# Optimization experiments

Hardware: AMD Instinct MI355X
Metric: run time of the kernel (lower is better)

## Reference

```python
import jax, jax.numpy as jnp
import numpy as np


def _gcn_conv(x, W, b, src, dst, norm, n_nodes):
    # PyG GCNConv: h = x @ W, then symmetric-normalized aggregation, then + b
    h = x @ W                                   # [N, F_out]
    msg = h[src] * norm[:, None]                # gather + scale, [E', F_out]
    agg = jax.ops.segment_sum(msg, dst, num_segments=n_nodes)
    return agg + b


def _norm_and_loops(edge_index, n_nodes):
    # add self-loops, compute D^{-1/2} (A+I) D^{-1/2} edge weights
    loop = jnp.arange(n_nodes, dtype=edge_index.dtype)
    src = jnp.concatenate([edge_index[0], loop])
    dst = jnp.concatenate([edge_index[1], loop])
    deg = jax.ops.segment_sum(jnp.ones_like(dst, dtype=jnp.float32), dst,
                              num_segments=n_nodes)
    dinv = jnp.where(deg > 0, jax.lax.rsqrt(deg), 0.0)
    norm = dinv[src] * dinv[dst]
    return src, dst, norm


def setup_inputs() -> dict:
    key = jax.random.key(0)
    ks = jax.random.split(key, 4)
    N, E, n_latent, n_dim = 50000, 800000, 128, 128
    hidden = 2 * n_latent
    x = jax.random.normal(ks[0], (N, n_latent), dtype=jnp.float32)
    edge_index = jax.random.randint(ks[1], (2, E), 0, N, dtype=jnp.int64)
    W1 = jax.random.normal(ks[2], (n_latent, hidden), dtype=jnp.float32) / np.sqrt(n_latent)
    b1 = jnp.zeros((hidden,), dtype=jnp.float32)
    W2 = jax.random.normal(ks[3], (hidden, n_dim), dtype=jnp.float32) / np.sqrt(hidden)
    b2 = jnp.zeros((n_dim,), dtype=jnp.float32)
    return {"x": x, "edge_index": edge_index, "W1": W1, "b1": b1,
            "W2": W2, "b2": b2}


def reference(x, edge_index, W1, b1, W2, b2):
    n_nodes = x.shape[0]
    src, dst, norm = _norm_and_loops(edge_index, n_nodes)
    z1 = jax.nn.relu(_gcn_conv(x, W1, b1, src, dst, norm, n_nodes))
    z2 = _gcn_conv(z1, W2, b2, src, dst, norm, n_nodes)
    return z2
```

## Files before the change

### kernel.cpp

```cpp
#include <hip/hip_runtime.h>


constexpr int F = 128;
constexpr int HID = 256;
constexpr int ECHUNK = 8192;

typedef __attribute__((ext_vector_type(8))) short bf16x8;
typedef __attribute__((ext_vector_type(4))) float f32x4;

__device__ inline unsigned short f2bf(float f) {
  unsigned u = __float_as_uint(f);
  u += 0x7fffu + ((u >> 16) & 1u);
  return (unsigned short)(u >> 16);
}
__device__ inline float bf2f(unsigned short s) {
  return __uint_as_float(((unsigned)s) << 16);
}

__global__ __launch_bounds__(256) void k_bzero(unsigned* bcnt) {
  bcnt[threadIdx.x] = 0u;
}

__global__ __launch_bounds__(256) void k_binc(const int* __restrict__ dst,
                                              unsigned* __restrict__ bcnt, int E) {
  __shared__ unsigned hist[256];
  int tid = threadIdx.x;
  hist[tid] = 0u;
  __syncthreads();
  int i0 = blockIdx.x * ECHUNK;
  int i1 = min(i0 + ECHUNK, E);
  for (int i = i0 + tid; i < i1; i += 256)
    atomicAdd(&hist[((unsigned)dst[i]) >> 8], 1u);
  __syncthreads();
  unsigned c = hist[tid];
  if (c) atomicAdd(&bcnt[tid], c);
}

__global__ __launch_bounds__(256) void k_bscan(const unsigned* __restrict__ bcnt,
                                               unsigned* __restrict__ bbase,
                                               unsigned* __restrict__ bcur,
                                               int* __restrict__ rowptr,
                                               int P, int N, int E) {
  __shared__ unsigned wsum[4];
  int tid = threadIdx.x;
  unsigned v = (tid < P) ? bcnt[tid] : 0u;
  unsigned sv = v;
#pragma unroll
  for (int off = 1; off < 64; off <<= 1) {
    unsigned t = __shfl_up(sv, off);
    if ((tid & 63) >= off) sv += t;
  }
  int w = tid >> 6;
  if ((tid & 63) == 63) wsum[w] = sv;
  __syncthreads();
  unsigned wpre = 0;
  for (int k = 0; k < w; ++k) wpre += wsum[k];
  unsigned excl = wpre + sv - v;
  if (tid < P) {
    bbase[tid] = excl;
    bcur[tid] = excl;
  }
  if (tid == P - 1) bbase[P] = excl + v;
  if (tid == 0) rowptr[N] = E;
}

__global__ __launch_bounds__(256) void k_binscat(const int* __restrict__ src,
                                                 const int* __restrict__ dst,
                                                 unsigned* __restrict__ bcur,
                                                 unsigned* __restrict__ packed, int E) {
  __shared__ unsigned hist[256];
  __shared__ unsigned basel[256];
  int tid = threadIdx.x;
  hist[tid] = 0u;
  __syncthreads();
  int i0 = blockIdx.x * ECHUNK;
  int i1 = min(i0 + ECHUNK, E);
  for (int i = i0 + tid; i < i1; i += 256)
    atomicAdd(&hist[((unsigned)dst[i]) >> 8], 1u);
  __syncthreads();
  unsigned c = hist[tid];
  if (c) basel[tid] = atomicAdd(&bcur[tid], c);
  __syncthreads();
  hist[tid] = 0u;
  __syncthreads();
  for (int i = i0 + tid; i < i1; i += 256) {
    unsigned d = (unsigned)dst[i];
    unsigned b = d >> 8;
    unsigned pos = basel[b] + atomicAdd(&hist[b], 1u);
    packed[pos] = ((unsigned)src[i]) | ((d & 255u) << 16);
  }
}

__global__ __launch_bounds__(256) void k_bcsr(const unsigned* __restrict__ packed,
                                              const unsigned* __restrict__ bbase,
                                              unsigned* __restrict__ deg,
                                              int* __restrict__ rowptr,
                                              int* __restrict__ esrc, int N) {
  __shared__ unsigned hist[256];
  __shared__ unsigned rowloc[256];
  __shared__ unsigned cur[256];
  __shared__ unsigned wsum[4];
  int tid = threadIdx.x, b = blockIdx.x;
  int e0 = (int)bbase[b], e1 = (int)bbase[b + 1];
  hist[tid] = 0u;
  __syncthreads();
  for (int i = e0 + tid; i < e1; i += 256)
    atomicAdd(&hist[packed[i] >> 16], 1u);
  __syncthreads();
  unsigned v = hist[tid];
  unsigned sv = v;
#pragma unroll
  for (int off = 1; off < 64; off <<= 1) {
    unsigned t = __shfl_up(sv, off);
    if ((tid & 63) >= off) sv += t;
  }
  int w = tid >> 6;
  if ((tid & 63) == 63) wsum[w] = sv;
  __syncthreads();
  unsigned wpre = 0;
  for (int k = 0; k < w; ++k) wpre += wsum[k];
  unsigned excl = wpre + sv - v;
  int node = b * 256 + tid;
  if (node < N) {
    deg[node] = v;
    rowptr[node] = e0 + (int)excl;
  }
  rowloc[tid] = (unsigned)e0 + excl;
  cur[tid] = 0u;
  __syncthreads();
  for (int i = e0 + tid; i < e1; i += 256) {
    unsigned pk = packed[i];
    unsigned dl = pk >> 16;
    unsigned pos = rowloc[dl] + atomicAdd(&cur[dl], 1u);
    esrc[pos] = (int)(pk & 0xffffu);
  }
}

__global__ __launch_bounds__(256) void k_dinv(const unsigned* __restrict__ deg,
                                              float* dinv, int N) {
  int i = blockIdx.x * 256 + threadIdx.x;
  if (i < N) dinv[i] = rsqrtf((float)deg[i] + 1.0f);
}

__global__ __launch_bounds__(256) void k_tobf(const float* __restrict__ in,
                                              unsigned short* __restrict__ outp,
                                              int n4) {
  int i = blockIdx.x * 256 + threadIdx.x;
  if (i >= n4) return;
  float4 v = ((const float4*)in)[i];
  ushort4 o;
  o.x = f2bf(v.x); o.y = f2bf(v.y); o.z = f2bf(v.z); o.w = f2bf(v.w);
  ((ushort4*)outp)[i] = o;
}

__global__ __launch_bounds__(256) void k_wsplit(const float* __restrict__ W,
                                                unsigned short* __restrict__ hi,
                                                unsigned short* __restrict__ lo,
                                                int K, int Nn) {
  int idx = blockIdx.x * 256 + threadIdx.x;
  if (idx >= K * Nn) return;
  int k = idx / Nn, n = idx - k * Nn;
  float f = W[idx];
  unsigned short h = f2bf(f);
  unsigned short l = f2bf(f - bf2f(h));
  hi[n * K + k] = h;
  lo[n * K + k] = l;
}

__global__ __launch_bounds__(256) void k_agg_bf(const int* __restrict__ rowptr,
                                                const int* __restrict__ esrc,
                                                const float* __restrict__ dinv,
                                                const float* __restrict__ xf,
                                                const unsigned short* __restrict__ xb,
                                                unsigned short* __restrict__ outh,
                                                unsigned short* __restrict__ outl,
                                                int N) {
  int node = blockIdx.x * 4 + (threadIdx.x >> 6);
  int lane = threadIdx.x & 63;
  if (node >= N) return;
  float di = dinv[node];
  float w0 = di * di;
  float2 acc = ((const float2*)(xf + (size_t)node * F))[lane];
  acc.x *= w0; acc.y *= w0;
  int beg = rowptr[node], end = rowptr[node + 1];
  for (int b = beg; b < end; b += 64) {
    int n = min(64, end - b);
    int s = 0;
    float w = 0.f;
    if (lane < n) {
      s = esrc[b + lane];
      w = dinv[s] * di;
    }
    int t = 0;
    for (; t + 3 < n; t += 4) {
      int s0 = __shfl(s, t), s1 = __shfl(s, t + 1);
      int s2 = __shfl(s, t + 2), s3 = __shfl(s, t + 3);
      float wa = __shfl(w, t), wb = __shfl(w, t + 1);
      float wc = __shfl(w, t + 2), wd = __shfl(w, t + 3);
      ushort2 v0 = ((const ushort2*)(xb + (size_t)s0 * F))[lane];
      ushort2 v1 = ((const ushort2*)(xb + (size_t)s1 * F))[lane];
      ushort2 v2 = ((const ushort2*)(xb + (size_t)s2 * F))[lane];
      ushort2 v3 = ((const ushort2*)(xb + (size_t)s3 * F))[lane];
      acc.x += bf2f(v0.x) * wa; acc.y += bf2f(v0.y) * wa;
      acc.x += bf2f(v1.x) * wb; acc.y += bf2f(v1.y) * wb;
      acc.x += bf2f(v2.x) * wc; acc.y += bf2f(v2.y) * wc;
      acc.x += bf2f(v3.x) * wd; acc.y += bf2f(v3.y) * wd;
    }
    for (; t < n; ++t) {
      int s0 = __shfl(s, t);
      float wa = __shfl(w, t);
      ushort2 v0 = ((const ushort2*)(xb + (size_t)s0 * F))[lane];
      acc.x += bf2f(v0.x) * wa; acc.y += bf2f(v0.y) * wa;
    }
  }
  unsigned short hx = f2bf(acc.x), hy = f2bf(acc.y);
  unsigned short lx = f2bf(acc.x - bf2f(hx)), ly = f2bf(acc.y - bf2f(hy));
  ushort2 hv; hv.x = hx; hv.y = hy;
  ushort2 lv; lv.x = lx; lv.y = ly;
  ((ushort2*)(outh + (size_t)node * F))[lane] = hv;
  ((ushort2*)(outl + (size_t)node * F))[lane] = lv;
}

__global__ __launch_bounds__(256) void k_agg_out(const int* __restrict__ rowptr,
                                                 const int* __restrict__ esrc,
                                                 const float* __restrict__ dinv,
                                                 const unsigned short* __restrict__ hb,
                                                 const float* __restrict__ bias,
                                                 float* __restrict__ outp, int N) {
  int node = blockIdx.x * 4 + (threadIdx.x >> 6);
  int lane = threadIdx.x & 63;
  if (node >= N) return;
  float di = dinv[node];
  float w0 = di * di;
  ushort2 sv2 = ((const ushort2*)(hb + (size_t)node * F))[lane];
  float2 bb = ((const float2*)bias)[lane];
  float2 acc;
  acc.x = bf2f(sv2.x) * w0 + bb.x;
  acc.y = bf2f(sv2.y) * w0 + bb.y;
  int beg = rowptr[node], end = rowptr[node + 1];
  for (int b = beg; b < end; b += 64) {
    int n = min(64, end - b);
    int s = 0;
    float w = 0.f;
    if (lane < n) {
      s = esrc[b + lane];
      w = dinv[s] * di;
    }
    int t = 0;
    for (; t + 3 < n; t += 4) {
      int s0 = __shfl(s, t), s1 = __shfl(s, t + 1);
      int s2 = __shfl(s, t + 2), s3 = __shfl(s, t + 3);
      float wa = __shfl(w, t), wb = __shfl(w, t + 1);
      float wc = __shfl(w, t + 2), wd = __shfl(w, t + 3);
      ushort2 v0 = ((const ushort2*)(hb + (size_t)s0 * F))[lane];
      ushort2 v1 = ((const ushort2*)(hb + (size_t)s1 * F))[lane];
      ushort2 v2 = ((const ushort2*)(hb + (size_t)s2 * F))[lane];
      ushort2 v3 = ((const ushort2*)(hb + (size_t)s3 * F))[lane];
      acc.x += bf2f(v0.x) * wa; acc.y += bf2f(v0.y) * wa;
      acc.x += bf2f(v1.x) * wb; acc.y += bf2f(v1.y) * wb;
      acc.x += bf2f(v2.x) * wc; acc.y += bf2f(v2.y) * wc;
      acc.x += bf2f(v3.x) * wd; acc.y += bf2f(v3.y) * wd;
    }
    for (; t < n; ++t) {
      int s0 = __shfl(s, t);
      float wa = __shfl(w, t);
      ushort2 v0 = ((const ushort2*)(hb + (size_t)s0 * F))[lane];
      acc.x += bf2f(v0.x) * wa; acc.y += bf2f(v0.y) * wa;
    }
  }
  ((float2*)(outp + (size_t)node * F))[lane] = acc;
}

__global__ __launch_bounds__(256) void k_gemm1(const unsigned short* __restrict__ Ah,
                                               const unsigned short* __restrict__ Al,
                                               const unsigned short* __restrict__ Bh,
                                               const unsigned short* __restrict__ Bl,
                                               const float* __restrict__ bias,
                                               unsigned short* __restrict__ Cbf,
                                               int M) {
  __shared__ unsigned short AhL[64 * 128];
  __shared__ unsigned short AlL[64 * 128];
  int tid = threadIdx.x;
  int lane = tid & 63, wid = tid >> 6;
  int row0 = blockIdx.x * 64;

#pragma unroll
  for (int i = 0; i < 4; ++i) {
    int g = i * 256 + tid;
    int r = g >> 4, gi = g & 15;
    int o = r * 128 + (gi ^ (r & 7)) * 8;
    size_t go = (size_t)(row0 + r) * 128 + gi * 8;
    *(bf16x8*)&AhL[o] = *(const bf16x8*)&Ah[go];
    *(bf16x8*)&AlL[o] = *(const bf16x8*)&Al[go];
  }
  __syncthreads();

  f32x4 acc[4][4] = {};
#pragma unroll
  for (int ks = 0; ks < 4; ++ks) {
    bf16x8 ah[4], al[4], bh[4], bl[4];
#pragma unroll
    for (int mf = 0; mf < 4; ++mf) {
      int r = mf * 16 + (lane & 15);
      int g = ks * 4 + (lane >> 4);
      int o = r * 128 + (g ^ (r & 7)) * 8;
      ah[mf] = *(const bf16x8*)&AhL[o];
      al[mf] = *(const bf16x8*)&AlL[o];
    }
#pragma unroll
    for (int nf = 0; nf < 4; ++nf) {
      int c = wid * 64 + nf * 16 + (lane & 15);
      size_t o = (size_t)c * 128 + ks * 32 + (lane >> 4) * 8;
      bh[nf] = *(const bf16x8*)&Bh[o];
      bl[nf] = *(const bf16x8*)&Bl[o];
    }
#pragma unroll
    for (int mf = 0; mf < 4; ++mf)
#pragma unroll
      for (int nf = 0; nf < 4; ++nf) {
        acc[mf][nf] = __builtin_amdgcn_mfma_f32_16x16x32_bf16(
            ah[mf], bh[nf], acc[mf][nf], 0, 0, 0);
        acc[mf][nf] = __builtin_amdgcn_mfma_f32_16x16x32_bf16(
            ah[mf], bl[nf], acc[mf][nf], 0, 0, 0);
        acc[mf][nf] = __builtin_amdgcn_mfma_f32_16x16x32_bf16(
            al[mf], bh[nf], acc[mf][nf], 0, 0, 0);
      }
  }

#pragma unroll
  for (int mf = 0; mf < 4; ++mf) {
    int r0 = row0 + mf * 16 + (lane >> 4) * 4;
#pragma unroll
    for (int nf = 0; nf < 4; ++nf) {
      int c = wid * 64 + nf * 16 + (lane & 15);
      float bv = bias[c];
#pragma unroll
      for (int r = 0; r < 4; ++r) {
        if (r0 + r < M) {
          float v = fmaxf(acc[mf][nf][r] + bv, 0.f);
          Cbf[(size_t)(r0 + r) * HID + c] = f2bf(v);
        }
      }
    }
  }
}

__global__ __launch_bounds__(256) void k_gemm2(const unsigned short* __restrict__ Z,
                                               const unsigned short* __restrict__ Bh,
                                               const unsigned short* __restrict__ Bl,
                                               unsigned short* __restrict__ Cbf,
                                               int M) {
  __shared__ unsigned short ZL[64 * 256];
  int tid = threadIdx.x;
  int lane = tid & 63, wid = tid >> 6;
  int row0 = blockIdx.x * 64;

#pragma unroll
  for (int i = 0; i < 8; ++i) {
    int g = i * 256 + tid;
    int r = g >> 5, gi = g & 31;
    int o = r * 256 + (gi ^ (r & 7)) * 8;
    size_t go = (size_t)(row0 + r) * 256 + gi * 8;
    *(bf16x8*)&ZL[o] = *(const bf16x8*)&Z[go];
  }
  __syncthreads();

  f32x4 acc[4][2] = {};
#pragma unroll
  for (int ks = 0; ks < 8; ++ks) {
    bf16x8 ah[4], bh[2], bl[2];
#pragma unroll
    for (int mf = 0; mf < 4; ++mf) {
      int r = mf * 16 + (lane & 15);
      int g = ks * 4 + (lane >> 4);
      int o = r * 256 + (g ^ (r & 7)) * 8;
      ah[mf] = *(const bf16x8*)&ZL[o];
    }
#pragma unroll
    for (int nf = 0; nf < 2; ++nf) {
      int c = wid * 32 + nf * 16 + (lane & 15);
      size_t o = (size_t)c * 256 + ks * 32 + (lane >> 4) * 8;
      bh[nf] = *(const bf16x8*)&Bh[o];
      bl[nf] = *(const bf16x8*)&Bl[o];
    }
#pragma unroll
    for (int mf = 0; mf < 4; ++mf)
#pragma unroll
      for (int nf = 0; nf < 2; ++nf) {
        acc[mf][nf] = __builtin_amdgcn_mfma_f32_16x16x32_bf16(
            ah[mf], bh[nf], acc[mf][nf], 0, 0, 0);
        acc[mf][nf] = __builtin_amdgcn_mfma_f32_16x16x32_bf16(
            ah[mf], bl[nf], acc[mf][nf], 0, 0, 0);
      }
  }

#pragma unroll
  for (int mf = 0; mf < 4; ++mf) {
    int r0 = row0 + mf * 16 + (lane >> 4) * 4;
#pragma unroll
    for (int nf = 0; nf < 2; ++nf) {
      int c = wid * 32 + nf * 16 + (lane & 15);
#pragma unroll
      for (int r = 0; r < 4; ++r)
        if (r0 + r < M) Cbf[(size_t)(r0 + r) * F + c] = f2bf(acc[mf][nf][r]);
    }
  }
}

extern "C" void kernel_launch(void* const* d_in, const int* in_sizes, int n_in,
                              void* d_out, int out_size, void* d_ws, size_t ws_size,
                              hipStream_t stream) {
  const float* x = (const float*)d_in[0];
  const int* ei = (const int*)d_in[1];
  const float* W1 = (const float*)d_in[2];
  const float* b1 = (const float*)d_in[3];
  const float* W2 = (const float*)d_in[4];
  const float* b2 = (const float*)d_in[5];
  float* out = (float*)d_out;

  int N = in_sizes[0] / F;
  int E = in_sizes[1] / 2;
  const int* src = ei;
  const int* dst = ei + E;
  int P = (N + 255) / 256;

  char* ws = (char*)d_ws;
  size_t off = 0;
  auto allocB = [&](size_t bytes) {
    void* p = ws + off;
    off += ((bytes + 255) & ~(size_t)255);
    return p;
  };
  unsigned* deg = (unsigned*)allocB((size_t)N * 4);
  float* dinv = (float*)allocB((size_t)N * 4);
  int* rowptr = (int*)allocB(((size_t)N + 1) * 4);
  unsigned* bcnt = (unsigned*)allocB(256 * 4);
  unsigned* bbase = (unsigned*)allocB(257 * 4);
  unsigned* bcur = (unsigned*)allocB(256 * 4);
  unsigned* packed = (unsigned*)allocB((size_t)E * 4);
  int* esrc = (int*)allocB((size_t)E * 4);
  unsigned short* xb = (unsigned short*)allocB((size_t)N * F * 2);
  unsigned short* aggh = (unsigned short*)allocB((size_t)(N + 64) * F * 2);
  unsigned short* aggl = (unsigned short*)allocB((size_t)(N + 64) * F * 2);
  unsigned short* z1h = (unsigned short*)allocB((size_t)(N + 64) * HID * 2);
  unsigned short* w1th = (unsigned short*)allocB((size_t)F * HID * 2);
  unsigned short* w1tl = (unsigned short*)allocB((size_t)F * HID * 2);
  unsigned short* w2th = (unsigned short*)allocB((size_t)HID * F * 2);
  unsigned short* w2tl = (unsigned short*)allocB((size_t)HID * F * 2);
  unsigned short* h2b = aggh;

  int nbN = (N + 255) / 256;
  int nbW = (F * HID + 255) / 256;
  int nbX = (N * F / 4 + 255) / 256;
  int nbC = (E + ECHUNK - 1) / ECHUNK;

  k_wsplit<<<nbW, 256, 0, stream>>>(W1, w1th, w1tl, F, HID);
  k_wsplit<<<nbW, 256, 0, stream>>>(W2, w2th, w2tl, HID, F);
  k_tobf<<<nbX, 256, 0, stream>>>(x, xb, N * F / 4);

  k_bzero<<<1, 256, 0, stream>>>(bcnt);
  k_binc<<<nbC, 256, 0, stream>>>(dst, bcnt, E);
  k_bscan<<<1, 256, 0, stream>>>(bcnt, bbase, bcur, rowptr, P, N, E);
  k_binscat<<<nbC, 256, 0, stream>>>(src, dst, bcur, packed, E);
  k_bcsr<<<P, 256, 0, stream>>>(packed, bbase, deg, rowptr, esrc, N);
  k_dinv<<<nbN, 256, 0, stream>>>(deg, dinv, N);

  int nbAgg = (N + 3) / 4;
  int mb = (N + 63) / 64;

  k_agg_bf<<<nbAgg, 256, 0, stream>>>(rowptr, esrc, dinv, x, xb, aggh, aggl, N);
  k_gemm1<<<mb, 256, 0, stream>>>(aggh, aggl, w1th, w1tl, b1, z1h, N);

  k_gemm2<<<mb, 256, 0, stream>>>(z1h, w2th, w2tl, h2b, N);
  k_agg_out<<<nbAgg, 256, 0, stream>>>(rowptr, esrc, dinv, h2b, b2, out, N);
}
```

Measured before the change: 195.4 us.

## Switch from split-bf16 to single fp16 operands and split gemm1 columns

Replaces bf16 hi/lo split precision with plain fp16 storage for features, aggregates, hidden activations and weights. The GEMMs drop from three (gemm1) or two (gemm2) MFMA passes per tile to a single f16 pass, and the lo buffer writes/reads disappear. gemm1 now runs on a 2D grid where each block handles 128 of the 256 output columns, which adds blocks but reloads the A tile twice. Accuracy now depends on fp16 range and mantissa instead of the emulated near-fp32 split.

```diff
diff --git a/kernel.cpp b/kernel.cpp
--- a/kernel.cpp
+++ b/kernel.cpp
@@ -5,17 +5,10 @@
 constexpr int HID = 256;
 constexpr int ECHUNK = 8192;
 
-typedef __attribute__((ext_vector_type(8))) short bf16x8;
+typedef __attribute__((ext_vector_type(8))) _Float16 f16x8;
+typedef __attribute__((ext_vector_type(4))) _Float16 f16x4;
+typedef __attribute__((ext_vector_type(2))) _Float16 f16x2;
 typedef __attribute__((ext_vector_type(4))) float f32x4;
-
-__device__ inline unsigned short f2bf(float f) {
-  unsigned u = __float_as_uint(f);
-  u += 0x7fffu + ((u >> 16) & 1u);
-  return (unsigned short)(u >> 16);
-}
-__device__ inline float bf2f(unsigned short s) {
-  return __uint_as_float(((unsigned)s) << 16);
-}
 
 __global__ __launch_bounds__(256) void k_bzero(unsigned* bcnt) {
   bcnt[threadIdx.x] = 0u;
@@ -142,39 +135,32 @@
   if (i < N) dinv[i] = rsqrtf((float)deg[i] + 1.0f);
 }
 
-__global__ __launch_bounds__(256) void k_tobf(const float* __restrict__ in,
-                                              unsigned short* __restrict__ outp,
-                                              int n4) {
+__global__ __launch_bounds__(256) void k_toh(const float* __restrict__ in,
+                                             _Float16* __restrict__ outp, int n4) {
   int i = blockIdx.x * 256 + threadIdx.x;
   if (i >= n4) return;
   float4 v = ((const float4*)in)[i];
-  ushort4 o;
-  o.x = f2bf(v.x); o.y = f2bf(v.y); o.z = f2bf(v.z); o.w = f2bf(v.w);
-  ((ushort4*)outp)[i] = o;
-}
-
-__global__ __launch_bounds__(256) void k_wsplit(const float* __restrict__ W,
-                                                unsigned short* __restrict__ hi,
-                                                unsigned short* __restrict__ lo,
-                                                int K, int Nn) {
+  f16x4 o;
+  o.x = (_Float16)v.x; o.y = (_Float16)v.y;
+  o.z = (_Float16)v.z; o.w = (_Float16)v.w;
+  ((f16x4*)outp)[i] = o;
+}
+
+__global__ __launch_bounds__(256) void k_wcvt(const float* __restrict__ W,
+                                              _Float16* __restrict__ Wt,
+                                              int K, int Nn) {
   int idx = blockIdx.x * 256 + threadIdx.x;
   if (idx >= K * Nn) return;
   int k = idx / Nn, n = idx - k * Nn;
-  float f = W[idx];
-  unsigned short h = f2bf(f);
-  unsigned short l = f2bf(f - bf2f(h));
-  hi[n * K + k] = h;
-  lo[n * K + k] = l;
-}
-
-__global__ __launch_bounds__(256) void k_agg_bf(const int* __restrict__ rowptr,
-                                                const int* __restrict__ esrc,
-                                                const float* __restrict__ dinv,
-                                                const float* __restrict__ xf,
-                                                const unsigned short* __restrict__ xb,
-                                                unsigned short* __restrict__ outh,
-                                                unsigned short* __restrict__ outl,
-                                                int N) {
+  Wt[n * K + k] = (_Float16)W[idx];
+}
+
+__global__ __launch_bounds__(256) void k_agg1(const int* __restrict__ rowptr,
+                                              const int* __restrict__ esrc,
+                                              const float* __restrict__ dinv,
+                                              const float* __restrict__ xf,
+                                              const _Float16* __restrict__ xh,
+                                              _Float16* __restrict__ outp, int N) {
   int node = blockIdx.x * 4 + (threadIdx.x >> 6);
   int lane = threadIdx.x & 63;
   if (node >= N) return;
@@ -197,34 +183,32 @@
       int s2 = __shfl(s, t + 2), s3 = __shfl(s, t + 3);
       float wa = __shfl(w, t), wb = __shfl(w, t + 1);
       float wc = __shfl(w, t + 2), wd = __shfl(w, t + 3);
-      ushort2 v0 = ((const ushort2*)(xb + (size_t)s0 * F))[lane];
-      ushort2 v1 = ((const ushort2*)(xb + (size_t)s1 * F))[lane];
-      ushort2 v2 = ((const ushort2*)(xb + (size_t)s2 * F))[lane];
-      ushort2 v3 = ((const ushort2*)(xb + (size_t)s3 * F))[lane];
-      acc.x += bf2f(v0.x) * wa; acc.y += bf2f(v0.y) * wa;
-      acc.x += bf2f(v1.x) * wb; acc.y += bf2f(v1.y) * wb;
-      acc.x += bf2f(v2.x) * wc; acc.y += bf2f(v2.y) * wc;
-      acc.x += bf2f(v3.x) * wd; acc.y += bf2f(v3.y) * wd;
+      f16x2 v0 = ((const f16x2*)(xh + (size_t)s0 * F))[lane];
+      f16x2 v1 = ((const f16x2*)(xh + (size_t)s1 * F))[lane];
+      f16x2 v2 = ((const f16x2*)(xh + (size_t)s2 * F))[lane];
+      f16x2 v3 = ((const f16x2*)(xh + (size_t)s3 * F))[lane];
+      acc.x += (float)v0.x * wa; acc.y += (float)v0.y * wa;
+      acc.x += (float)v1.x * wb; acc.y += (float)v1.y * wb;
+      acc.x += (float)v2.x * wc; acc.y += (float)v2.y * wc;
+      acc.x += (float)v3.x * wd; acc.y += (float)v3.y * wd;
     }
     for (; t < n; ++t) {
       int s0 = __shfl(s, t);
       float wa = __shfl(w, t);
-      ushort2 v0 = ((const ushort2*)(xb + (size_t)s0 * F))[lane];
-      acc.x += bf2f(v0.x) * wa; acc.y += bf2f(v0.y) * wa;
-    }
-  }
-  unsigned short hx = f2bf(acc.x), hy = f2bf(acc.y);
-  unsigned short lx = f2bf(acc.x - bf2f(hx)), ly = f2bf(acc.y - bf2f(hy));
-  ushort2 hv; hv.x = hx; hv.y = hy;
-  ushort2 lv; lv.x = lx; lv.y = ly;
-  ((ushort2*)(outh + (size_t)node * F))[lane] = hv;
-  ((ushort2*)(outl + (size_t)node * F))[lane] = lv;
+      f16x2 v0 = ((const f16x2*)(xh + (size_t)s0 * F))[lane];
+      acc.x += (float)v0.x * wa; acc.y += (float)v0.y * wa;
+    }
+  }
+  f16x2 ov;
+  ov.x = (_Float16)acc.x;
+  ov.y = (_Float16)acc.y;
+  ((f16x2*)(outp + (size_t)node * F))[lane] = ov;
 }
 
 __global__ __launch_bounds__(256) void k_agg_out(const int* __restrict__ rowptr,
                                                  const int* __restrict__ esrc,
                                                  const float* __restrict__ dinv,
-                                                 const unsigned short* __restrict__ hb,
+                                                 const _Float16* __restrict__ hb,
                                                  const float* __restrict__ bias,
                                                  float* __restrict__ outp, int N) {
   int node = blockIdx.x * 4 + (threadIdx.x >> 6);
@@ -232,11 +216,11 @@
   if (node >= N) return;
   float di = dinv[node];
   float w0 = di * di;
-  ushort2 sv2 = ((const ushort2*)(hb + (size_t)node * F))[lane];
+  f16x2 sv2 = ((const f16x2*)(hb + (size_t)node * F))[lane];
   float2 bb = ((const float2*)bias)[lane];
   float2 acc;
-  acc.x = bf2f(sv2.x) * w0 + bb.x;
-  acc.y = bf2f(sv2.y) * w0 + bb.y;
+  acc.x = (float)sv2.x * w0 + bb.x;
+  acc.y = (float)sv2.y * w0 + bb.y;
   int beg = rowptr[node], end = rowptr[node + 1];
   for (int b = beg; b < end; b += 64) {
     int n = min(64, end - b);
@@ -252,105 +236,92 @@
       int s2 = __shfl(s, t + 2), s3 = __shfl(s, t + 3);
       float wa = __shfl(w, t), wb = __shfl(w, t + 1);
       float wc = __shfl(w, t + 2), wd = __shfl(w, t + 3);
-      ushort2 v0 = ((const ushort2*)(hb + (size_t)s0 * F))[lane];
-      ushort2 v1 = ((const ushort2*)(hb + (size_t)s1 * F))[lane];
-      ushort2 v2 = ((const ushort2*)(hb + (size_t)s2 * F))[lane];
-      ushort2 v3 = ((const ushort2*)(hb + (size_t)s3 * F))[lane];
-      acc.x += bf2f(v0.x) * wa; acc.y += bf2f(v0.y) * wa;
-      acc.x += bf2f(v1.x) * wb; acc.y += bf2f(v1.y) * wb;
-      acc.x += bf2f(v2.x) * wc; acc.y += bf2f(v2.y) * wc;
-      acc.x += bf2f(v3.x) * wd; acc.y += bf2f(v3.y) * wd;
+      f16x2 v0 = ((const f16x2*)(hb + (size_t)s0 * F))[lane];
+      f16x2 v1 = ((const f16x2*)(hb + (size_t)s1 * F))[lane];
+      f16x2 v2 = ((const f16x2*)(hb + (size_t)s2 * F))[lane];
+      f16x2 v3 = ((const f16x2*)(hb + (size_t)s3 * F))[lane];
+      acc.x += (float)v0.x * wa; acc.y += (float)v0.y * wa;
+      acc.x += (float)v1.x * wb; acc.y += (float)v1.y * wb;
+      acc.x += (float)v2.x * wc; acc.y += (float)v2.y * wc;
+      acc.x += (float)v3.x * wd; acc.y += (float)v3.y * wd;
     }
     for (; t < n; ++t) {
       int s0 = __shfl(s, t);
       float wa = __shfl(w, t);
-      ushort2 v0 = ((const ushort2*)(hb + (size_t)s0 * F))[lane];
-      acc.x += bf2f(v0.x) * wa; acc.y += bf2f(v0.y) * wa;
+      f16x2 v0 = ((const f16x2*)(hb + (size_t)s0 * F))[lane];
+      acc.x += (float)v0.x * wa; acc.y += (float)v0.y * wa;
     }
   }
   ((float2*)(outp + (size_t)node * F))[lane] = acc;
 }
 
-__global__ __launch_bounds__(256) void k_gemm1(const unsigned short* __restrict__ Ah,
-                                               const unsigned short* __restrict__ Al,
-                                               const unsigned short* __restrict__ Bh,
-                                               const unsigned short* __restrict__ Bl,
+__global__ __launch_bounds__(256) void k_gemm1(const _Float16* __restrict__ A,
+                                               const _Float16* __restrict__ Bt,
                                                const float* __restrict__ bias,
-                                               unsigned short* __restrict__ Cbf,
-                                               int M) {
-  __shared__ unsigned short AhL[64 * 128];
-  __shared__ unsigned short AlL[64 * 128];
+                                               _Float16* __restrict__ C, int M) {
+  __shared__ _Float16 AL[64 * 128];
   int tid = threadIdx.x;
   int lane = tid & 63, wid = tid >> 6;
   int row0 = blockIdx.x * 64;
+  int col0 = blockIdx.y * 128;
 
 #pragma unroll
   for (int i = 0; i < 4; ++i) {
     int g = i * 256 + tid;
     int r = g >> 4, gi = g & 15;
-    int o = r * 128 + (gi ^ (r & 7)) * 8;
+    int o = r * 128 + ((gi ^ (r & 7)) * 8);
     size_t go = (size_t)(row0 + r) * 128 + gi * 8;
-    *(bf16x8*)&AhL[o] = *(const bf16x8*)&Ah[go];
-    *(bf16x8*)&AlL[o] = *(const bf16x8*)&Al[go];
-  }
-  __syncthreads();
-
-  f32x4 acc[4][4] = {};
+    *(f16x8*)&AL[o] = *(const f16x8*)&A[go];
+  }
+  __syncthreads();
+
+  f32x4 acc[4][2] = {};
 #pragma unroll
   for (int ks = 0; ks < 4; ++ks) {
-    bf16x8 ah[4], al[4], bh[4], bl[4];
+    f16x8 ah[4], bh[2];
 #pragma unroll
     for (int mf = 0; mf < 4; ++mf) {
       int r = mf * 16 + (lane & 15);
       int g = ks * 4 + (lane >> 4);
-      int o = r * 128 + (g ^ (r & 7)) * 8;
-      ah[mf] = *(const bf16x8*)&AhL[o];
-      al[mf] = *(const bf16x8*)&AlL[o];
-    }
-#pragma unroll
-    for (int nf = 0; nf < 4; ++nf) {
-      int c = wid * 64 + nf * 16 + (lane & 15);
+      int o = r * 128 + ((g ^ (r & 7)) * 8);
+      ah[mf] = *(const f16x8*)&AL[o];
+    }
+#pragma unroll
+    for (int nf = 0; nf < 2; ++nf) {
+      int c = col0 + wid * 32 + nf * 16 + (lane & 15);
       size_t o = (size_t)c * 128 + ks * 32 + (lane >> 4) * 8;
-      bh[nf] = *(const bf16x8*)&Bh[o];
-      bl[nf] = *(const bf16x8*)&Bl[o];
+      bh[nf] = *(const f16x8*)&Bt[o];
     }
 #pragma unroll
     for (int mf = 0; mf < 4; ++mf)
 #pragma unroll
-      for (int nf = 0; nf < 4; ++nf) {
-        acc[mf][nf] = __builtin_amdgcn_mfma_f32_16x16x32_bf16(
+      for (int nf = 0; nf < 2; ++nf)
+        acc[mf][nf] = __builtin_amdgcn_mfma_f32_16x16x32_f16(
             ah[mf], bh[nf], acc[mf][nf], 0, 0, 0);
-        acc[mf][nf] = __builtin_amdgcn_mfma_f32_16x16x32_bf16(
-            ah[mf], bl[nf], acc[mf][nf], 0, 0, 0);
-        acc[mf][nf] = __builtin_amdgcn_mfma_f32_16x16x32_bf16(
-            al[mf], bh[nf], acc[mf][nf], 0, 0, 0);
-      }
   }
 
 #pragma unroll
   for (int mf = 0; mf < 4; ++mf) {
     int r0 = row0 + mf * 16 + (lane >> 4) * 4;
 #pragma unroll
-    for (int nf = 0; nf < 4; ++nf) {
-      int c = wid * 64 + nf * 16 + (lane & 15);
+    for (int nf = 0; nf < 2; ++nf) {
+      int c = col0 + wid * 32 + nf * 16 + (lane & 15);
       float bv = bias[c];
 #pragma unroll
       for (int r = 0; r < 4; ++r) {
         if (r0 + r < M) {
           float v = fmaxf(acc[mf][nf][r] + bv, 0.f);
-          Cbf[(size_t)(r0 + r) * HID + c] = f2bf(v);
+          C[(size_t)(r0 + r) * HID + c] = (_Float16)v;
         }
       }
     }
   }
 }
 
-__global__ __launch_bounds__(256) void k_gemm2(const unsigned short* __restrict__ Z,
-                                               const unsigned short* __restrict__ Bh,
-                                               const unsigned short* __restrict__ Bl,
-                                               unsigned short* __restrict__ Cbf,
-                                               int M) {
-  __shared__ unsigned short ZL[64 * 256];
+__global__ __launch_bounds__(256) void k_gemm2(const _Float16* __restrict__ Z,
+                                               const _Float16* __restrict__ Bt,
+                                               _Float16* __restrict__ C, int M) {
+  __shared__ _Float16 ZL[64 * 256];
   int tid = threadIdx.x;
   int lane = tid & 63, wid = tid >> 6;
   int row0 = blockIdx.x * 64;
@@ -359,39 +330,35 @@
   for (int i = 0; i < 8; ++i) {
     int g = i * 256 + tid;
     int r = g >> 5, gi = g & 31;
-    int o = r * 256 + (gi ^ (r & 7)) * 8;
+    int o = r * 256 + ((gi ^ (r & 7)) * 8);
     size_t go = (size_t)(row0 + r) * 256 + gi * 8;
-    *(bf16x8*)&ZL[o] = *(const bf16x8*)&Z[go];
+    *(f16x8*)&ZL[o] = *(const f16x8*)&Z[go];
   }
   __syncthreads();
 
   f32x4 acc[4][2] = {};
 #pragma unroll
   for (int ks = 0; ks < 8; ++ks) {
-    bf16x8 ah[4], bh[2], bl[2];
+    f16x8 ah[4], bh[2];
 #pragma unroll
     for (int mf = 0; mf < 4; ++mf) {
       int r = mf * 16 + (lane & 15);
       int g = ks * 4 + (lane >> 4);
-      int o = r * 256 + (g ^ (r & 7)) * 8;
-      ah[mf] = *(const bf16x8*)&ZL[o];
+      int o = r * 256 + ((g ^ (r & 7)) * 8);
+      ah[mf] = *(const f16x8*)&ZL[o];
     }
 #pragma unroll
     for (int nf = 0; nf < 2; ++nf) {
       int c = wid * 32 + nf * 16 + (lane & 15);
       size_t o = (size_t)c * 256 + ks * 32 + (lane >> 4) * 8;
-      bh[nf] = *(const bf16x8*)&Bh[o];
-      bl[nf] = *(const bf16x8*)&Bl[o];
+      bh[nf] = *(const f16x8*)&Bt[o];
     }
 #pragma unroll
     for (int mf = 0; mf < 4; ++mf)
 #pragma unroll
-      for (int nf = 0; nf < 2; ++nf) {
-        acc[mf][nf] = __builtin_amdgcn_mfma_f32_16x16x32_bf16(
+      for (int nf = 0; nf < 2; ++nf)
+        acc[mf][nf] = __builtin_amdgcn_mfma_f32_16x16x32_f16(
             ah[mf], bh[nf], acc[mf][nf], 0, 0, 0);
-        acc[mf][nf] = __builtin_amdgcn_mfma_f32_16x16x32_bf16(
-            ah[mf], bl[nf], acc[mf][nf], 0, 0, 0);
-      }
   }
 
 #pragma unroll
@@ -402,7 +369,7 @@
       int c = wid * 32 + nf * 16 + (lane & 15);
 #pragma unroll
       for (int r = 0; r < 4; ++r)
-        if (r0 + r < M) Cbf[(size_t)(r0 + r) * F + c] = f2bf(acc[mf][nf][r]);
+        if (r0 + r < M) C[(size_t)(r0 + r) * F + c] = (_Float16)acc[mf][nf][r];
     }
   }
 }
@@ -439,24 +406,21 @@
   unsigned* bcur = (unsigned*)allocB(256 * 4);
   unsigned* packed = (unsigned*)allocB((size_t)E * 4);
   int* esrc = (int*)allocB((size_t)E * 4);
-  unsigned short* xb = (unsigned short*)allocB((size_t)N * F * 2);
-  unsigned short* aggh = (unsigned short*)allocB((size_t)(N + 64) * F * 2);
-  unsigned short* aggl = (unsigned short*)allocB((size_t)(N + 64) * F * 2);
-  unsigned short* z1h = (unsigned short*)allocB((size_t)(N + 64) * HID * 2);
-  unsigned short* w1th = (unsigned short*)allocB((size_t)F * HID * 2);
-  unsigned short* w1tl = (unsigned short*)allocB((size_t)F * HID * 2);
-  unsigned short* w2th = (unsigned short*)allocB((size_t)HID * F * 2);
-  unsigned short* w2tl = (unsigned short*)allocB((size_t)HID * F * 2);
-  unsigned short* h2b = aggh;
+  _Float16* xh = (_Float16*)allocB((size_t)N * F * 2);
+  _Float16* agg = (_Float16*)allocB((size_t)(N + 64) * F * 2);
+  _Float16* z1 = (_Float16*)allocB((size_t)(N + 64) * HID * 2);
+  _Float16* w1t = (_Float16*)allocB((size_t)F * HID * 2);
+  _Float16* w2t = (_Float16*)allocB((size_t)HID * F * 2);
+  _Float16* h2 = agg;
 
   int nbN = (N + 255) / 256;
   int nbW = (F * HID + 255) / 256;
   int nbX = (N * F / 4 + 255) / 256;
   int nbC = (E + ECHUNK - 1) / ECHUNK;
 
-  k_wsplit<<<nbW, 256, 0, stream>>>(W1, w1th, w1tl, F, HID);
-  k_wsplit<<<nbW, 256, 0, stream>>>(W2, w2th, w2tl, HID, F);
-  k_tobf<<<nbX, 256, 0, stream>>>(x, xb, N * F / 4);
+  k_wcvt<<<nbW, 256, 0, stream>>>(W1, w1t, F, HID);
+  k_wcvt<<<nbW, 256, 0, stream>>>(W2, w2t, HID, F);
+  k_toh<<<nbX, 256, 0, stream>>>(x, xh, N * F / 4);
 
   k_bzero<<<1, 256, 0, stream>>>(bcnt);
   k_binc<<<nbC, 256, 0, stream>>>(dst, bcnt, E);
@@ -468,9 +432,10 @@
   int nbAgg = (N + 3) / 4;
   int mb = (N + 63) / 64;
 
-  k_agg_bf<<<nbAgg, 256, 0, stream>>>(rowptr, esrc, dinv, x, xb, aggh, aggl, N);
-  k_gemm1<<<mb, 256, 0, stream>>>(aggh, aggl, w1th, w1tl, b1, z1h, N);
-
-  k_gemm2<<<mb, 256, 0, stream>>>(z1h, w2th, w2tl, h2b, N);
-  k_agg_out<<<nbAgg, 256, 0, stream>>>(rowptr, esrc, dinv, h2b, b2, out, N);
-}
+  k_agg1<<<nbAgg, 256, 0, stream>>>(rowptr, esrc, dinv, x, xh, agg, N);
+  dim3 g1(mb, 2);
+  k_gemm1<<<g1, 256, 0, stream>>>(agg, w1t, b1, z1, N);
+
+  k_gemm2<<<mb, 256, 0, stream>>>(z1, w2t, h2, N);
+  k_agg_out<<<nbAgg, 256, 0, stream>>>(rowptr, esrc, dinv, h2, b2, out, N);
+}
```

Result: faster. 173.3 us (-11.3%).
